# Optimization experiments

Measured on AMD Instinct MI355X. Metric: run time of the kernel, lower is better.

The kernel has to match this reference:

```python
import jax, jax.numpy as jnp
import numpy as np

B = 2048    # graphs in batch
V = 15      # nodes per graph
T = 16      # window (args.n_his)
F_IN = 2    # num_features
H = 64      # nhid
LH = 40     # LSTM hidden per direction
EPER = 40   # edges per graph
N = B * V
E = B * EPER
EPS = 1e-5


def setup_inputs() -> dict:
    key = jax.random.key(0)
    ks = jax.random.split(key, 12)

    def rn(k, shape, fan_in):
        return jax.random.normal(k, shape, jnp.float32) / np.sqrt(fan_in).astype(np.float32)

    # block-diagonal batched edge_index (PyG-style batching of B graphs of V nodes)
    rng = np.random.default_rng(0)
    off = np.arange(B)[:, None] * V
    src = rng.integers(0, V, (B, EPER)) + off
    dst = rng.integers(0, V, (B, EPER)) + off
    edge_index = jnp.asarray(np.stack([src.ravel(), dst.ravel()]), dtype=jnp.int32)

    return {
        "data": jax.random.normal(ks[0], (N, F_IN, T), jnp.float32),
        "edge_attr": jax.random.uniform(ks[1], (E,), jnp.float32),
        "W1": rn(ks[2], (H, F_IN), F_IN), "b1": jnp.zeros((H,), jnp.float32),
        "Wg1": rn(ks[3], (H, H), H), "bg1": jnp.zeros((H,), jnp.float32),
        "gamma1": jnp.ones((H,), jnp.float32), "beta1": jnp.zeros((H,), jnp.float32),
        "Wg2": rn(ks[4], (H, H), H), "bg2": jnp.zeros((H,), jnp.float32),
        "gamma2": jnp.ones((H,), jnp.float32), "beta2": jnp.zeros((H,), jnp.float32),
        "Wf": rn(ks[5], (H, V * H), V * H), "bf": jnp.zeros((H,), jnp.float32),
        "Wih_f": rn(ks[6], (4 * LH, H), H), "Whh_f": rn(ks[7], (4 * LH, LH), LH),
        "bih_f": jnp.zeros((4 * LH,), jnp.float32), "bhh_f": jnp.zeros((4 * LH,), jnp.float32),
        "Wih_b": rn(ks[8], (4 * LH, H), H), "Whh_b": rn(ks[9], (4 * LH, LH), LH),
        "bih_b": jnp.zeros((4 * LH,), jnp.float32), "bhh_b": jnp.zeros((4 * LH,), jnp.float32),
        "Wc1": rn(ks[10], (16, 2 * LH), 2 * LH), "bc1": jnp.zeros((16,), jnp.float32),
        "Wc2": rn(ks[11], (1, 16), 16), "bc2": jnp.zeros((1,), jnp.float32),
        "edge_index": edge_index,
    }


def _gcn(x, W, b, edge_index, ew):
    # PyG GCNConv: linear, add self-loops (weight 1), symmetric D^-1/2 (A+I) D^-1/2.
    # x: [N, T, H] -- all T timesteps processed at once (vectorizes the source loop).
    row, col = edge_index[0], edge_index[1]
    loop = jnp.arange(N, dtype=edge_index.dtype)
    row_s = jnp.concatenate([row, loop])
    col_s = jnp.concatenate([col, loop])
    ew_s = jnp.concatenate([ew, jnp.ones((N,), ew.dtype)])
    deg = jax.ops.segment_sum(ew_s, col_s, num_segments=N)
    dinv = jnp.where(deg > 0, jax.lax.rsqrt(deg), 0.0)
    norm = dinv[row_s] * ew_s * dinv[col_s]                      # [E+N]
    xw = jnp.einsum('nth,hk->ntk', x, W)                          # [N, T, H]
    agg = jax.ops.segment_sum(norm[:, None, None] * xw[row_s], col_s, num_segments=N)
    return agg + b


def _bn(x, gamma, beta):
    # BatchNorm1d training-mode stats, per timestep (axis 0 = nodes), biased var.
    m = x.mean(axis=0)
    v = x.var(axis=0)
    return gamma * (x - m) * jax.lax.rsqrt(v + EPS) + beta


def _lstm(X, Wih, Whh, bih, bhh):
    # X: [T, B, H]; PyTorch gate order i, f, g, o.
    def step(carry, xt):
        h, c = carry
        g = xt @ Wih.T + h @ Whh.T + (bih + bhh)
        i, f, gg, o = jnp.split(g, 4, axis=-1)
        c = jax.nn.sigmoid(f) * c + jax.nn.sigmoid(i) * jnp.tanh(gg)
        h = jax.nn.sigmoid(o) * jnp.tanh(c)
        return (h, c), h
    h0 = jnp.zeros((X.shape[1], LH), X.dtype)
    _, hs = jax.lax.scan(step, (h0, h0), X)
    return hs


def _forward(data, edge_attr, W1, b1, Wg1, bg1, gamma1, beta1, Wg2, bg2, gamma2, beta2,
             Wf, bf, Wih_f, Whh_f, bih_f, bhh_f, Wih_b, Whh_b, bih_b, bhh_b,
             Wc1, bc1, Wc2, bc2, edge_index):
    # conv_1 (1x1 Conv2d) == per-node linear over features, kept per timestep
    x = jnp.einsum('nft,hf->nth', data, W1) + b1                 # [N, T, H]
    # Hierarchical GCN with residuals (ReLU then BN, per the source)
    x1 = _bn(jax.nn.relu(_gcn(x, Wg1, bg1, edge_index, edge_attr)), gamma1, beta1) + x
    x2 = _bn(jax.nn.relu(_gcn(x1, Wg2, bg2, edge_index, edge_attr)), gamma2, beta2) + x1
    # stack over timesteps -> [T, B, V*H]
    Xs = x2.transpose(1, 0, 2).reshape(T, B, V * H)
    Xs = jax.nn.relu(Xs @ Wf.T + bf)                             # fc1 -> [T, B, H]
    hs_f = _lstm(Xs, Wih_f, Whh_f, bih_f, bhh_f)
    hs_b = _lstm(Xs[::-1], Wih_b, Whh_b, bih_b, bhh_b)
    # r_out[-1] = [fwd h at t=T-1, bwd h at t=T-1 (first step of reversed scan)]
    last = jnp.concatenate([hs_f[-1], hs_b[0]], axis=-1)          # [B, 80]
    hcls = jax.nn.relu(last @ Wc1.T + bc1)                        # dropout inactive (eval)
    return hcls @ Wc2.T + bc2                                     # [B, 1]


def reference(data, edge_attr, W1, b1, Wg1, bg1, gamma1, beta1, Wg2, bg2, gamma2, beta2,
              Wf, bf, Wih_f, Whh_f, bih_f, bhh_f, Wih_b, Whh_b, bih_b, bhh_b,
              Wc1, bc1, Wc2, bc2, edge_index):
    return _forward(data, edge_attr, W1, b1, Wg1, bg1, gamma1, beta1, Wg2, bg2,
                    gamma2, beta2, Wf, bf, Wih_f, Whh_f, bih_f, bhh_f,
                    Wih_b, Whh_b, bih_b, bhh_b, Wc1, bc1, Wc2, bc2, edge_index)
```

## Files before the change

### kernel.cpp

```cpp
#include <hip/hip_runtime.h>

typedef unsigned int u32;
typedef unsigned short u16;
typedef __attribute__((ext_vector_type(8))) short bf16x8;
typedef __attribute__((ext_vector_type(4))) float f32x4;

#define NB   2048
#define NV   15
#define NT   16
#define NH   64
#define NLH  40
#define EPER 40
#define NN   (NB*NV)
#define NE   (NB*EPER)

#define F_DATA 0
#define F_EA   983040
#define P_W1   1064960
#define P_B1   1065088
#define P_WG1  1065152
#define P_BG1  1069248
#define P_G1   1069312
#define P_BE1  1069376
#define P_WG2  1069440
#define P_BG2  1073536
#define P_G2   1073600
#define P_BE2  1073664
#define P_WF   1073728
#define P_BF   1135168
#define P_WIHF 1135232
#define P_WHHF 1145472
#define P_BIHF 1151872
#define P_BHHF 1152032
#define P_WIHB 1152192
#define P_WHHB 1162432
#define P_BIHB 1168832
#define P_BHHB 1168992
#define P_WC1  1169152
#define P_BC1  1170432
#define P_WC2  1170448
#define P_BC2  1170464
#define CVT_TOTAL 1170465
#define WFB_OFF   1170496
#define WIHT_OFF  1205504
#define STATS_OFF 1231936
#define XS_OFF    1240128
#define FLAG_OFF  3337280
#define BUFX_BYTE 13349376
#define BUFY_BYTE 76263936

__device__ const int d_cum[27] = {
  0, 983040, 1064960, 1065088, 1065152, 1069248, 1069312, 1069376,
  1069440, 1073536, 1073600, 1073664, 1073728, 1135168, 1135232, 1145472,
  1151872, 1152032, 1152192, 1162432, 1168832, 1168992, 1169152, 1170432,
  1170448, 1170464, 1170465};

struct Ptrs { const void* p[26]; };

__device__ inline float b2f(u16 u) { return __uint_as_float(((u32)u) << 16); }
__device__ inline u16 f2b(float f) {
  u32 u = __float_as_uint(f);
  u32 r = (u + 0x7FFFu + ((u >> 16) & 1u)) >> 16;
  return (u16)r;
}
__device__ inline float sigf(float x) { return 1.0f / (1.0f + __expf(-x)); }

__global__ void k_detect(const u16* __restrict__ raw, int* __restrict__ flag) {
  __shared__ int bad;
  if (threadIdx.x == 0) bad = 0;
  __syncthreads();
  for (int i = threadIdx.x; i < 4096; i += 256) {
    float f = b2f(raw[i]);
    if (!(fabsf(f) < 1000.0f)) atomicOr(&bad, 1);
  }
  __syncthreads();
  if (threadIdx.x == 0) *flag = bad ? 0 : 1;
}

__global__ void k_convert(Ptrs ptrs, float* __restrict__ W) {
  int gid = blockIdx.x * 256 + threadIdx.x;
  if (gid >= CVT_TOTAL) return;
  int flag = *(const int*)(W + FLAG_OFF);
  int ti = 0;
  #pragma unroll
  for (int i = 1; i < 26; ++i) ti += (gid >= d_cum[i]);
  int j = gid - d_cum[ti];
  const void* src = ptrs.p[ti];
  W[gid] = flag ? b2f(((const u16*)src)[j]) : ((const float*)src)[j];
}

__global__ void k_conv1(const float* __restrict__ W, u16* __restrict__ bufX) {
  int gid = blockIdx.x * 256 + threadIdx.x;
  int h8 = gid & 7, t = (gid >> 3) & 15, n = gid >> 7;
  float d0 = W[F_DATA + n * 32 + t];
  float d1 = W[F_DATA + n * 32 + 16 + t];
  u32 out[4];
  #pragma unroll
  for (int jp = 0; jp < 4; ++jp) {
    int h = h8 * 8 + jp * 2;
    float v0 = fmaf(d0, W[P_W1 + h * 2],       fmaf(d1, W[P_W1 + h * 2 + 1],       W[P_B1 + h]));
    float v1 = fmaf(d0, W[P_W1 + (h + 1) * 2], fmaf(d1, W[P_W1 + (h + 1) * 2 + 1], W[P_B1 + h + 1]));
    out[jp] = (u32)f2b(v0) | ((u32)f2b(v1) << 16);
  }
  *reinterpret_cast<uint4*>(bufX + (size_t)gid * 8) = make_uint4(out[0], out[1], out[2], out[3]);
}

__global__ void k_preswz(float* __restrict__ W, u16* __restrict__ WfB) {
  int i = blockIdx.x * 256 + threadIdx.x;
  if (i < 61440) {
    int j = i & 7, lane = (i >> 3) & 63, kt = (i >> 9) & 3, ks = i >> 11;
    int kout = kt * 16 + (lane & 15);
    int m = ks * 32 + ((lane >> 4) << 3) + j;
    WfB[i] = f2b(W[P_WF + kout * 960 + m]);
  } else if (i < 69632) {
    int ii = i - 61440;
    int L = ii >> 12, r = ii & 4095;
    int j = r & 7, lane = (r >> 3) & 63, nt = (r >> 9) & 3, ks = (r >> 11) & 1;
    int h = ks * 32 + ((lane >> 4) << 3) + j;
    int k = nt * 16 + (lane & 15);
    WfB[i] = f2b(W[(L ? P_WG2 : P_WG1) + h * 64 + k]);
  } else if (i < 90112) {
    int e = i - 69632;
    int which = e / 10240, rem = e % 10240;
    int kk = rem / 160, jj = rem % 160;
    W[WIHT_OFF + e] = W[(which ? P_WIHB : P_WIHF) + jj * 64 + kk];
  }
}

template<int LAYER>
__global__ __launch_bounds__(256, 4)
void k_gcn(const float* __restrict__ W, const int* __restrict__ ei,
           const u16* __restrict__ bufIn, u16* __restrict__ bufRes,
           u16* __restrict__ bufOut, const u16* __restrict__ WgB,
           float* __restrict__ S1, float* __restrict__ S2,
           int bgoff, int scoff, int shoff) {
  __shared__ u16 s_x[15360];
  __shared__ float s_m[240];
  __shared__ float s_deg[16];
  __shared__ int s_row[40], s_col[40];

  int g = blockIdx.x, tid = threadIdx.x;
  float ew = 0.f; int er = 0, ec = 0;
  if (tid < 40) {
    er = ei[g * 40 + tid] - g * 15;
    ec = ei[NE + g * 40 + tid] - g * 15;
    ew = W[F_EA + g * 40 + tid];
    s_row[tid] = er; s_col[tid] = ec;
  }
  if (tid >= 64 && tid < 80) s_deg[tid - 64] = 1.0f;
  for (int i = tid; i < 240; i += 256) s_m[i] = 0.f;

  const u32* pin = (const u32*)(bufIn + g * 15360);
  u32* sx32 = (u32*)s_x;
  if (LAYER == 1) {
    #pragma unroll
    for (int c = 0; c < 30; ++c) {
      int i = tid + c * 256;
      int t = (i >> 5) & 15;
      sx32[(((u32)(i << 2)) ^ (((u32)(t & 7)) << 4)) >> 2] = pin[i];
    }
  } else {
    u32* pres = (u32*)(bufRes + g * 15360);
    #pragma unroll 2
    for (int c = 0; c < 30; ++c) {
      int i = tid + c * 256;
      u32 uy = pin[i], ux = pres[i];
      int th = (2 * i) & 1023;
      int t = th >> 6;
      float a = fmaf(b2f((u16)(uy & 0xffff)), W[scoff + th],     W[shoff + th])     + b2f((u16)(ux & 0xffff));
      float b = fmaf(b2f((u16)(uy >> 16)),    W[scoff + th + 1], W[shoff + th + 1]) + b2f((u16)(ux >> 16));
      u32 pk = (u32)f2b(a) | ((u32)f2b(b) << 16);
      pres[i] = pk;
      sx32[(((u32)(i << 2)) ^ (((u32)(t & 7)) << 4)) >> 2] = pk;
    }
  }
  __syncthreads();
  if (tid < 40) atomicAdd(&s_deg[ec], ew);
  __syncthreads();
  if (tid < 15) s_deg[tid] = rsqrtf(s_deg[tid]);
  __syncthreads();
  if (tid < 40) atomicAdd(&s_m[ec * 16 + er], s_deg[er] * ew * s_deg[ec]);
  if (tid >= 64 && tid < 80) {
    float dv = s_deg[tid - 64];
    atomicAdd(&s_m[(tid - 64) * 17], dv * dv);
  }
  __syncthreads();

  {
    float x0[15], x1[15], x2[15], x3[15];
    int p0 = tid, p1 = tid + 256;
    int t0 = p0 >> 5, h0 = (2 * p0) & 63;
    int t1 = p1 >> 5, h1 = (2 * p1) & 63;
    u32 ba0 = ((u32)(t0 * 128 + h0 * 2)) ^ (((u32)(t0 & 7)) << 4);
    u32 ba1 = ((u32)(t1 * 128 + h1 * 2)) ^ (((u32)(t1 & 7)) << 4);
    #pragma unroll
    for (int v = 0; v < 15; ++v) {
      u32 ua = sx32[(ba0 + v * 2048) >> 2];
      u32 ub = sx32[(ba1 + v * 2048) >> 2];
      x0[v] = b2f((u16)(ua & 0xffff)); x1[v] = b2f((u16)(ua >> 16));
      x2[v] = b2f((u16)(ub & 0xffff)); x3[v] = b2f((u16)(ub >> 16));
    }
    #pragma unroll
    for (int vc = 0; vc < 15; ++vc) {
      float a0 = 0.f, a1 = 0.f, a2 = 0.f, a3 = 0.f;
      #pragma unroll
      for (int vr = 0; vr < 15; ++vr) {
        float m = s_m[vc * 16 + vr];
        a0 = fmaf(m, x0[vr], a0); a1 = fmaf(m, x1[vr], a1);
        a2 = fmaf(m, x2[vr], a2); a3 = fmaf(m, x3[vr], a3);
      }
      sx32[(ba0 + vc * 2048) >> 2] = (u32)f2b(a0) | ((u32)f2b(a1) << 16);
      sx32[(ba1 + vc * 2048) >> 2] = (u32)f2b(a2) | ((u32)f2b(a3) << 16);
    }
  }
  __syncthreads();

  int wid = tid >> 6, lane = tid & 63;
  int tA = lane & 15, kg = lane >> 4;
  const bf16x8* wb = (const bf16x8*)WgB;
  bf16x8 bf0 = wb[(0 * 4 + wid) * 64 + lane];
  bf16x8 bf1 = wb[(1 * 4 + wid) * 64 + lane];
  int kout = wid * 16 + tA;
  float bias = W[bgoff + kout];
  f32x4 acc[15];
  #pragma unroll
  for (int v = 0; v < 15; ++v) acc[v] = (f32x4){0.f, 0.f, 0.f, 0.f};
  u32 sw = ((u32)(tA & 7)) << 4;
  #pragma unroll
  for (int v = 0; v < 15; ++v) {
    u32 bb = (u32)(v * 2048 + tA * 128 + kg * 16);
    bf16x8 a0 = *(const bf16x8*)(s_x + ((bb ^ sw) >> 1));
    bf16x8 a1 = *(const bf16x8*)(s_x + (((bb + 64) ^ sw) >> 1));
    acc[v] = __builtin_amdgcn_mfma_f32_16x16x32_bf16(a0, bf0, acc[v], 0, 0, 0);
    acc[v] = __builtin_amdgcn_mfma_f32_16x16x32_bf16(a1, bf1, acc[v], 0, 0, 0);
  }
  float s1r[4] = {0.f, 0.f, 0.f, 0.f}, s2r[4] = {0.f, 0.f, 0.f, 0.f};
  u16* pout = bufOut + g * 15360;
  #pragma unroll
  for (int v = 0; v < 15; ++v) {
    #pragma unroll
    for (int r = 0; r < 4; ++r) {
      float y = fmaxf(acc[v][r] + bias, 0.f);
      pout[v * 1024 + (kg * 4 + r) * 64 + kout] = f2b(y);
      s1r[r] += y; s2r[r] += y * y;
    }
  }
  #pragma unroll
  for (int r = 0; r < 4; ++r) {
    int idx = (kg * 4 + r) * 64 + kout;
    atomicAdd(&S1[idx], s1r[r]);
    atomicAdd(&S2[idx], s2r[r]);
  }
}

__global__ void k_finalize(float* __restrict__ W, int layer) {
  int i = blockIdx.x * 256 + threadIdx.x;
  if (i >= 1024) return;
  int base = STATS_OFF + (layer == 1 ? 0 : 2048);
  int scb  = STATS_OFF + (layer == 1 ? 4096 : 6144);
  float m   = W[base + i] * (1.0f / 30720.0f);
  float var = W[base + 1024 + i] * (1.0f / 30720.0f) - m * m;
  float istd = rsqrtf(var + 1e-5f);
  int h = i & 63;
  float gm = W[(layer == 1 ? P_G1 : P_G2) + h];
  float bt = W[(layer == 1 ? P_BE1 : P_BE2) + h];
  float sc = gm * istd;
  W[scb + i] = sc;
  W[scb + 1024 + i] = bt - m * sc;
}

__global__ __launch_bounds__(256, 4)
void k_fc1(const float* __restrict__ W, const u16* __restrict__ bufY2,
           const u16* __restrict__ bufX1, const u16* __restrict__ WfB,
           float* __restrict__ Xs) {
  __shared__ u16 s_x[15360];
  __shared__ float s_sc[1024], s_sh[1024];
  int g = blockIdx.x, tid = threadIdx.x;
  for (int i = tid; i < 1024; i += 256) {
    s_sc[i] = W[STATS_OFF + 6144 + i];
    s_sh[i] = W[STATS_OFF + 7168 + i];
  }
  __syncthreads();
  const u32* py = (const u32*)(bufY2 + g * 15360);
  const u32* px = (const u32*)(bufX1 + g * 15360);
  u32* sx32 = (u32*)s_x;
  for (int i = tid; i < 7680; i += 256) {
    u32 uy = py[i], ux = px[i];
    int e = 2 * i;
    int th = e & 1023;
    int t = th >> 6;
    float a = fmaf(b2f((u16)(uy & 0xffff)), s_sc[th],     s_sh[th])     + b2f((u16)(ux & 0xffff));
    float b = fmaf(b2f((u16)(uy >> 16)),    s_sc[th + 1], s_sh[th + 1]) + b2f((u16)(ux >> 16));
    u32 byte = ((u32)(e << 1)) ^ (((u32)(t & 7)) << 4);
    sx32[byte >> 2] = (u32)f2b(a) | ((u32)f2b(b) << 16);
  }
  __syncthreads();

  int wid = tid >> 6, lane = tid & 63;
  int tA = lane & 15, kg = lane >> 4;
  f32x4 acc = {0.f, 0.f, 0.f, 0.f};
  const bf16x8* wf = (const bf16x8*)WfB;
  #pragma unroll 2
  for (int ks = 0; ks < 30; ++ks) {
    int v = ks >> 1, half = ks & 1;
    u32 byte = (u32)(v * 2048 + tA * 128 + (half * 32 + kg * 8) * 2) ^ (((u32)(tA & 7)) << 4);
    bf16x8 afrag = *(const bf16x8*)(s_x + (byte >> 1));
    bf16x8 bfrag = wf[(ks * 4 + wid) * 64 + lane];
    acc = __builtin_amdgcn_mfma_f32_16x16x32_bf16(afrag, bfrag, acc, 0, 0, 0);
  }
  int kout = wid * 16 + (lane & 15);
  float bias = W[P_BF + kout];
  #pragma unroll
  for (int r = 0; r < 4; ++r) {
    int t = (lane >> 4) * 4 + r;
    Xs[t * 131072 + g * 64 + kout] = fmaxf(acc[r] + bias, 0.0f);
  }
}

__global__ __launch_bounds__(256)
void k_gatex(const float* __restrict__ W, const float* __restrict__ Xs,
             float* __restrict__ gxf, float* __restrict__ gxb) {
  __shared__ float s_x[2048];
  __shared__ float s_w[10240];
  __shared__ float s_b[160];
  int blk = blockIdx.x, tid = threadIdx.x;
  int fwd = blk < 1024;
  const float* xsrc = fwd ? (Xs + blk * 2048) : (Xs + 1966080 + (blk - 1024) * 2048);
  const float* wsrc = W + WIHT_OFF + (fwd ? 0 : 10240);
  int bo  = fwd ? P_BIHF : P_BIHB;
  int bo2 = fwd ? P_BHHF : P_BHHB;
  float* out = fwd ? (gxf + blk * 5120) : (gxb + (blk - 1024) * 5120);

  float4* sx4 = (float4*)s_x;
  const float4* xs4 = (const float4*)xsrc;
  for (int i = tid; i < 512; i += 256) sx4[i] = xs4[i];
  for (int i = tid; i < 10240; i += 256) s_w[i] = wsrc[i];
  if (tid < 160) s_b[tid] = W[bo + tid] + W[bo2 + tid];
  __syncthreads();

  int rb = (tid >> 5) * 4, c0 = tid & 31;
  float acc[4][5];
  #pragma unroll
  for (int r = 0; r < 4; ++r)
    #pragma unroll
    for (int q = 0; q < 5; ++q) acc[r][q] = s_b[c0 + 32 * q];
  #pragma unroll 4
  for (int kk = 0; kk < 64; ++kk) {
    float w0 = s_w[kk * 160 + c0],      w1 = s_w[kk * 160 + c0 + 32];
    float w2 = s_w[kk * 160 + c0 + 64], w3 = s_w[kk * 160 + c0 + 96];
    float w4 = s_w[kk * 160 + c0 + 128];
    #pragma unroll
    for (int r = 0; r < 4; ++r) {
      float xv = s_x[(rb + r) * 64 + kk];
      acc[r][0] = fmaf(xv, w0, acc[r][0]);
      acc[r][1] = fmaf(xv, w1, acc[r][1]);
      acc[r][2] = fmaf(xv, w2, acc[r][2]);
      acc[r][3] = fmaf(xv, w3, acc[r][3]);
      acc[r][4] = fmaf(xv, w4, acc[r][4]);
    }
  }
  #pragma unroll
  for (int r = 0; r < 4; ++r)
    #pragma unroll
    for (int q = 0; q < 5; ++q)
      out[(rb + r) * 160 + c0 + 32 * q] = acc[r][q];
}

__global__ __launch_bounds__(512)
void k_lstm2(const float* __restrict__ W, const float* __restrict__ gxf,
             const float* __restrict__ gxb, void* __restrict__ dout,
             const int* __restrict__ flagp) {
  __shared__ float s_whh[40 * 162];
  __shared__ float s_h[320], s_c[320], s_hb[320];
  __shared__ float s_g[1280];
  __shared__ float s_cls[128];
  int tid = threadIdx.x, r0 = blockIdx.x * 8;

  for (int i = tid; i < 6400; i += 512) {
    int jj = i / 40, kk = i % 40;
    s_whh[kk * 162 + jj] = W[P_WHHF + i];
  }
  if (tid < 320) { s_h[tid] = 0.f; s_c[tid] = 0.f; }
  __syncthreads();

  int r = tid >> 6, l = tid & 63;
  int l2 = (l < 32) ? l + 128 : l;
  const float* gbase = gxf + (r0 + r) * 160;
  float g0 = gbase[l], g1 = gbase[l + 64], g2 = gbase[l2];

  for (int t = 0; t < 16; ++t) {
    float acc0 = g0, acc1 = g1, acc2 = g2;
    int tn = (t < 15) ? t + 1 : 15;
    const float* gnext = gbase + tn * 327680;
    g0 = gnext[l]; g1 = gnext[l + 64]; g2 = gnext[l2];
    const float* hr = s_h + r * 40;
    #pragma unroll 8
    for (int kk = 0; kk < 40; ++kk) {
      float hv = hr[kk];
      acc0 = fmaf(hv, s_whh[kk * 162 + l], acc0);
      acc1 = fmaf(hv, s_whh[kk * 162 + l + 64], acc1);
      acc2 = fmaf(hv, s_whh[kk * 162 + l2], acc2);
    }
    s_g[r * 160 + l] = acc0;
    s_g[r * 160 + l + 64] = acc1;
    if (l < 32) s_g[r * 160 + l2] = acc2;
    __syncthreads();
    if (tid < 320) {
      int row = tid / 40, jj = tid % 40;
      const float* gr = s_g + row * 160;
      float ig = gr[jj], fg = gr[jj + 40], gg = gr[jj + 80], og = gr[jj + 120];
      float c = sigf(fg) * s_c[tid] + sigf(ig) * tanhf(gg);
      s_c[tid] = c;
      s_h[tid] = sigf(og) * tanhf(c);
    }
    __syncthreads();
  }

  if (tid < 320) {
    int row = tid / 40, jj = tid % 40;
    const float* gb = gxb + (r0 + row) * 160;
    float ig = gb[jj], gg = gb[jj + 80], og = gb[jj + 120];
    float c = sigf(ig) * tanhf(gg);
    s_hb[tid] = sigf(og) * tanhf(c);
  }
  __syncthreads();

  if (tid < 128) {
    int rr = tid >> 4, jj = tid & 15;
    float a = W[P_BC1 + jj];
    for (int p = 0; p < 40; ++p) a = fmaf(W[P_WC1 + jj * 80 + p],      s_h[rr * 40 + p],  a);
    for (int p = 0; p < 40; ++p) a = fmaf(W[P_WC1 + jj * 80 + 40 + p], s_hb[rr * 40 + p], a);
    s_cls[rr * 16 + jj] = fmaxf(a, 0.0f);
  }
  __syncthreads();
  if (tid < 8) {
    float o = W[P_BC2];
    #pragma unroll
    for (int jj = 0; jj < 16; ++jj) o = fmaf(W[P_WC2 + jj], s_cls[tid * 16 + jj], o);
    if (*flagp) ((u16*)dout)[r0 + tid] = f2b(o);
    else        ((float*)dout)[r0 + tid] = o;
  }
}

extern "C" void kernel_launch(void* const* d_in, const int* in_sizes, int n_in,
                              void* d_out, int out_size, void* d_ws, size_t ws_size,
                              hipStream_t stream) {
  float* W = (float*)d_ws;
  u16* bufX = (u16*)((char*)d_ws + BUFX_BYTE);
  u16* bufY = (u16*)((char*)d_ws + BUFY_BYTE);
  u16* WfB  = (u16*)(W + WFB_OFF);
  float* gxf = (float*)((char*)d_ws + BUFX_BYTE);
  float* gxb = gxf + 5242880;
  const int* ei = (const int*)d_in[26];

  hipMemsetAsync(W + STATS_OFF, 0, 4096 * sizeof(float), stream);
  k_detect<<<1, 256, 0, stream>>>((const u16*)d_in[0], (int*)(W + FLAG_OFF));
  Ptrs ptrs;
  for (int i = 0; i < 26; ++i) ptrs.p[i] = d_in[i];
  k_convert<<<(CVT_TOTAL + 255) / 256, 256, 0, stream>>>(ptrs, W);
  k_preswz<<<352, 256, 0, stream>>>(W, WfB);
  k_conv1<<<NN * 16 * 8 / 256, 256, 0, stream>>>(W, bufX);
  k_gcn<1><<<NB, 256, 0, stream>>>(W, ei, bufX, nullptr, bufY, WfB + 61440,
      W + STATS_OFF, W + STATS_OFF + 1024, P_BG1, 0, 0);
  k_finalize<<<4, 256, 0, stream>>>(W, 1);
  k_gcn<2><<<NB, 256, 0, stream>>>(W, ei, bufY, bufX, bufY, WfB + 65536,
      W + STATS_OFF + 2048, W + STATS_OFF + 3072, P_BG2,
      STATS_OFF + 4096, STATS_OFF + 5120);
  k_finalize<<<4, 256, 0, stream>>>(W, 2);
  k_fc1<<<NB, 256, 0, stream>>>(W, bufY, bufX, WfB, W + XS_OFF);
  k_gatex<<<1088, 256, 0, stream>>>(W, W + XS_OFF, gxf, gxb);
  k_lstm2<<<256, 512, 0, stream>>>(W, gxf, gxb, d_out, (const int*)(W + FLAG_OFF));
}
```

Before: 377.5 us.

## Fuse input projection into GCN and fc1, recompute residuals instead of storing

Removes the separate conv1 kernel and the bf16 residual buffer. The input linear projection is recomputed from the raw data inside each GCN block and inside fc1, and the first-layer residual is rebuilt from stored pre-BN outputs plus BN scale/shift. This drops one kernel launch and several full-size global reads and writes of activation buffers. In exchange each block does a little more arithmetic and reads more per-element scale/shift vectors from global memory.

```diff
diff --git a/kernel.cpp b/kernel.cpp
--- a/kernel.cpp
+++ b/kernel.cpp
@@ -89,22 +89,6 @@
   W[gid] = flag ? b2f(((const u16*)src)[j]) : ((const float*)src)[j];
 }
 
-__global__ void k_conv1(const float* __restrict__ W, u16* __restrict__ bufX) {
-  int gid = blockIdx.x * 256 + threadIdx.x;
-  int h8 = gid & 7, t = (gid >> 3) & 15, n = gid >> 7;
-  float d0 = W[F_DATA + n * 32 + t];
-  float d1 = W[F_DATA + n * 32 + 16 + t];
-  u32 out[4];
-  #pragma unroll
-  for (int jp = 0; jp < 4; ++jp) {
-    int h = h8 * 8 + jp * 2;
-    float v0 = fmaf(d0, W[P_W1 + h * 2],       fmaf(d1, W[P_W1 + h * 2 + 1],       W[P_B1 + h]));
-    float v1 = fmaf(d0, W[P_W1 + (h + 1) * 2], fmaf(d1, W[P_W1 + (h + 1) * 2 + 1], W[P_B1 + h + 1]));
-    out[jp] = (u32)f2b(v0) | ((u32)f2b(v1) << 16);
-  }
-  *reinterpret_cast<uint4*>(bufX + (size_t)gid * 8) = make_uint4(out[0], out[1], out[2], out[3]);
-}
-
 __global__ void k_preswz(float* __restrict__ W, u16* __restrict__ WfB) {
   int i = blockIdx.x * 256 + threadIdx.x;
   if (i < 61440) {
@@ -130,14 +114,15 @@
 template<int LAYER>
 __global__ __launch_bounds__(256, 4)
 void k_gcn(const float* __restrict__ W, const int* __restrict__ ei,
-           const u16* __restrict__ bufIn, u16* __restrict__ bufRes,
-           u16* __restrict__ bufOut, const u16* __restrict__ WgB,
+           const u16* __restrict__ bufIn, u16* __restrict__ bufOut,
+           const u16* __restrict__ WgB,
            float* __restrict__ S1, float* __restrict__ S2,
            int bgoff, int scoff, int shoff) {
   __shared__ u16 s_x[15360];
   __shared__ float s_m[240];
   __shared__ float s_deg[16];
-  __shared__ int s_row[40], s_col[40];
+  __shared__ float s_d[480];
+  __shared__ float s_w1[192];
 
   int g = blockIdx.x, tid = threadIdx.x;
   float ew = 0.f; int er = 0, ec = 0;
@@ -145,37 +130,48 @@
     er = ei[g * 40 + tid] - g * 15;
     ec = ei[NE + g * 40 + tid] - g * 15;
     ew = W[F_EA + g * 40 + tid];
-    s_row[tid] = er; s_col[tid] = ec;
-  }
-  if (tid >= 64 && tid < 80) s_deg[tid - 64] = 1.0f;
+  }
+  if (tid >= 40 && tid < 56) s_deg[tid - 40] = 1.0f;
   for (int i = tid; i < 240; i += 256) s_m[i] = 0.f;
-
-  const u32* pin = (const u32*)(bufIn + g * 15360);
-  u32* sx32 = (u32*)s_x;
-  if (LAYER == 1) {
-    #pragma unroll
-    for (int c = 0; c < 30; ++c) {
-      int i = tid + c * 256;
-      int t = (i >> 5) & 15;
-      sx32[(((u32)(i << 2)) ^ (((u32)(t & 7)) << 4)) >> 2] = pin[i];
-    }
-  } else {
-    u32* pres = (u32*)(bufRes + g * 15360);
-    #pragma unroll 2
-    for (int c = 0; c < 30; ++c) {
-      int i = tid + c * 256;
-      u32 uy = pin[i], ux = pres[i];
-      int th = (2 * i) & 1023;
-      int t = th >> 6;
-      float a = fmaf(b2f((u16)(uy & 0xffff)), W[scoff + th],     W[shoff + th])     + b2f((u16)(ux & 0xffff));
-      float b = fmaf(b2f((u16)(uy >> 16)),    W[scoff + th + 1], W[shoff + th + 1]) + b2f((u16)(ux >> 16));
-      u32 pk = (u32)f2b(a) | ((u32)f2b(b) << 16);
-      pres[i] = pk;
-      sx32[(((u32)(i << 2)) ^ (((u32)(t & 7)) << 4)) >> 2] = pk;
-    }
-  }
-  __syncthreads();
+  if (tid >= 64 && tid < 184) ((float4*)s_d)[tid - 64] = ((const float4*)(W + F_DATA + g * 480))[tid - 64];
+  if (tid >= 192 && tid < 240) ((float4*)s_w1)[tid - 192] = ((const float4*)(W + P_W1))[tid - 192];
+  __syncthreads();
+
   if (tid < 40) atomicAdd(&s_deg[ec], ew);
+  for (int i = tid; i < 1920; i += 256) {
+    int v = i >> 7, rem = i & 127, t = rem >> 3, q = rem & 7;
+    int h0 = q * 8;
+    float d0 = s_d[v * 32 + t], d1 = s_d[v * 32 + 16 + t];
+    u32 pk[4];
+    if (LAYER == 1) {
+      #pragma unroll
+      for (int jp = 0; jp < 4; ++jp) {
+        int h = h0 + jp * 2;
+        float xa = fmaf(d0, s_w1[2 * h],     fmaf(d1, s_w1[2 * h + 1], s_w1[128 + h]));
+        float xb = fmaf(d0, s_w1[2 * h + 2], fmaf(d1, s_w1[2 * h + 3], s_w1[129 + h]));
+        pk[jp] = (u32)f2b(xa) | ((u32)f2b(xb) << 16);
+      }
+    } else {
+      uint4 uy = ((const uint4*)(bufIn + g * 15360))[i];
+      u32 uys[4] = {uy.x, uy.y, uy.z, uy.w};
+      int th0 = t * 64 + h0;
+      float4 A0 = *(const float4*)(W + scoff + th0), A1 = *(const float4*)(W + scoff + th0 + 4);
+      float4 B0 = *(const float4*)(W + shoff + th0), B1 = *(const float4*)(W + shoff + th0 + 4);
+      float scs[8] = {A0.x, A0.y, A0.z, A0.w, A1.x, A1.y, A1.z, A1.w};
+      float shs[8] = {B0.x, B0.y, B0.z, B0.w, B1.x, B1.y, B1.z, B1.w};
+      #pragma unroll
+      for (int jp = 0; jp < 4; ++jp) {
+        int j0 = jp * 2, h = h0 + j0;
+        float xa = fmaf(d0, s_w1[2 * h],     fmaf(d1, s_w1[2 * h + 1], s_w1[128 + h]));
+        float xb = fmaf(d0, s_w1[2 * h + 2], fmaf(d1, s_w1[2 * h + 3], s_w1[129 + h]));
+        float a = fmaf(b2f((u16)(uys[jp] & 0xffff)), scs[j0],     shs[j0])     + xa;
+        float b = fmaf(b2f((u16)(uys[jp] >> 16)),    scs[j0 + 1], shs[j0 + 1]) + xb;
+        pk[jp] = (u32)f2b(a) | ((u32)f2b(b) << 16);
+      }
+    }
+    u32 byte = ((u32)(i * 16)) ^ (((u32)(t & 7)) << 4);
+    *(uint4*)((char*)s_x + byte) = make_uint4(pk[0], pk[1], pk[2], pk[3]);
+  }
   __syncthreads();
   if (tid < 15) s_deg[tid] = rsqrtf(s_deg[tid]);
   __syncthreads();
@@ -186,6 +182,7 @@
   }
   __syncthreads();
 
+  u32* sx32 = (u32*)s_x;
   {
     float x0[15], x1[15], x2[15], x3[15];
     int p0 = tid, p1 = tid + 256;
@@ -271,28 +268,45 @@
 
 __global__ __launch_bounds__(256, 4)
 void k_fc1(const float* __restrict__ W, const u16* __restrict__ bufY2,
-           const u16* __restrict__ bufX1, const u16* __restrict__ WfB,
+           const u16* __restrict__ bufY1, const u16* __restrict__ WfB,
            float* __restrict__ Xs) {
   __shared__ u16 s_x[15360];
-  __shared__ float s_sc[1024], s_sh[1024];
+  __shared__ float s_d[480];
+  __shared__ float s_w1[192];
   int g = blockIdx.x, tid = threadIdx.x;
-  for (int i = tid; i < 1024; i += 256) {
-    s_sc[i] = W[STATS_OFF + 6144 + i];
-    s_sh[i] = W[STATS_OFF + 7168 + i];
-  }
-  __syncthreads();
-  const u32* py = (const u32*)(bufY2 + g * 15360);
-  const u32* px = (const u32*)(bufX1 + g * 15360);
-  u32* sx32 = (u32*)s_x;
-  for (int i = tid; i < 7680; i += 256) {
-    u32 uy = py[i], ux = px[i];
-    int e = 2 * i;
-    int th = e & 1023;
-    int t = th >> 6;
-    float a = fmaf(b2f((u16)(uy & 0xffff)), s_sc[th],     s_sh[th])     + b2f((u16)(ux & 0xffff));
-    float b = fmaf(b2f((u16)(uy >> 16)),    s_sc[th + 1], s_sh[th + 1]) + b2f((u16)(ux >> 16));
-    u32 byte = ((u32)(e << 1)) ^ (((u32)(t & 7)) << 4);
-    sx32[byte >> 2] = (u32)f2b(a) | ((u32)f2b(b) << 16);
+  if (tid < 120) ((float4*)s_d)[tid] = ((const float4*)(W + F_DATA + g * 480))[tid];
+  if (tid >= 128 && tid < 176) ((float4*)s_w1)[tid - 128] = ((const float4*)(W + P_W1))[tid - 128];
+  __syncthreads();
+  const uint4* py2 = (const uint4*)(bufY2 + g * 15360);
+  const uint4* py1 = (const uint4*)(bufY1 + g * 15360);
+  for (int i = tid; i < 1920; i += 256) {
+    int v = i >> 7, rem = i & 127, t = rem >> 3, q = rem & 7;
+    int h0 = q * 8, th0 = t * 64 + h0;
+    uint4 u2 = py2[i], u1 = py1[i];
+    u32 u2s[4] = {u2.x, u2.y, u2.z, u2.w}, u1s[4] = {u1.x, u1.y, u1.z, u1.w};
+    float d0 = s_d[v * 32 + t], d1 = s_d[v * 32 + 16 + t];
+    float4 A0 = *(const float4*)(W + STATS_OFF + 6144 + th0), A1 = *(const float4*)(W + STATS_OFF + 6148 + th0);
+    float4 B0 = *(const float4*)(W + STATS_OFF + 7168 + th0), B1 = *(const float4*)(W + STATS_OFF + 7172 + th0);
+    float4 C0 = *(const float4*)(W + STATS_OFF + 4096 + th0), C1 = *(const float4*)(W + STATS_OFF + 4100 + th0);
+    float4 D0 = *(const float4*)(W + STATS_OFF + 5120 + th0), D1 = *(const float4*)(W + STATS_OFF + 5124 + th0);
+    float sc2[8] = {A0.x, A0.y, A0.z, A0.w, A1.x, A1.y, A1.z, A1.w};
+    float sh2[8] = {B0.x, B0.y, B0.z, B0.w, B1.x, B1.y, B1.z, B1.w};
+    float sc1[8] = {C0.x, C0.y, C0.z, C0.w, C1.x, C1.y, C1.z, C1.w};
+    float sh1[8] = {D0.x, D0.y, D0.z, D0.w, D1.x, D1.y, D1.z, D1.w};
+    u32 pk[4];
+    #pragma unroll
+    for (int jp = 0; jp < 4; ++jp) {
+      int j0 = jp * 2, h = h0 + j0;
+      float xa = fmaf(d0, s_w1[2 * h],     fmaf(d1, s_w1[2 * h + 1], s_w1[128 + h]));
+      float xb = fmaf(d0, s_w1[2 * h + 2], fmaf(d1, s_w1[2 * h + 3], s_w1[129 + h]));
+      float x1a = fmaf(b2f((u16)(u1s[jp] & 0xffff)), sc1[j0],     sh1[j0])     + xa;
+      float x1b = fmaf(b2f((u16)(u1s[jp] >> 16)),    sc1[j0 + 1], sh1[j0 + 1]) + xb;
+      float a = fmaf(b2f((u16)(u2s[jp] & 0xffff)), sc2[j0],     sh2[j0])     + x1a;
+      float b = fmaf(b2f((u16)(u2s[jp] >> 16)),    sc2[j0 + 1], sh2[j0 + 1]) + x1b;
+      pk[jp] = (u32)f2b(a) | ((u32)f2b(b) << 16);
+    }
+    u32 byte = ((u32)(i * 16)) ^ (((u32)(t & 7)) << 4);
+    *(uint4*)((char*)s_x + byte) = make_uint4(pk[0], pk[1], pk[2], pk[3]);
   }
   __syncthreads();
 
@@ -459,15 +473,14 @@
   for (int i = 0; i < 26; ++i) ptrs.p[i] = d_in[i];
   k_convert<<<(CVT_TOTAL + 255) / 256, 256, 0, stream>>>(ptrs, W);
   k_preswz<<<352, 256, 0, stream>>>(W, WfB);
-  k_conv1<<<NN * 16 * 8 / 256, 256, 0, stream>>>(W, bufX);
-  k_gcn<1><<<NB, 256, 0, stream>>>(W, ei, bufX, nullptr, bufY, WfB + 61440,
+  k_gcn<1><<<NB, 256, 0, stream>>>(W, ei, nullptr, bufY, WfB + 61440,
       W + STATS_OFF, W + STATS_OFF + 1024, P_BG1, 0, 0);
   k_finalize<<<4, 256, 0, stream>>>(W, 1);
-  k_gcn<2><<<NB, 256, 0, stream>>>(W, ei, bufY, bufX, bufY, WfB + 65536,
+  k_gcn<2><<<NB, 256, 0, stream>>>(W, ei, bufY, bufX, WfB + 65536,
       W + STATS_OFF + 2048, W + STATS_OFF + 3072, P_BG2,
       STATS_OFF + 4096, STATS_OFF + 5120);
   k_finalize<<<4, 256, 0, stream>>>(W, 2);
-  k_fc1<<<NB, 256, 0, stream>>>(W, bufY, bufX, WfB, W + XS_OFF);
+  k_fc1<<<NB, 256, 0, stream>>>(W, bufX, bufY, WfB, W + XS_OFF);
   k_gatex<<<1088, 256, 0, stream>>>(W, W + XS_OFF, gxf, gxb);
   k_lstm2<<<256, 512, 0, stream>>>(W, gxf, gxb, d_out, (const int*)(W + FLAG_OFF));
 }
```

Measured after the change: 340.7 us. -9.7%, faster.
